# Kernel optimization log

Measured on AMD Instinct MI355X. Metric: run time of the kernel, lower is better.

## Reference

```python
import jax, jax.numpy as jnp
import numpy as np

DMODEL = 512
NUM_HEADS = 8
DK = DMODEL // NUM_HEADS  # 64
CAUSAL = True


def setup_inputs() -> dict:
    key = jax.random.key(0)
    ks = jax.random.split(key, 11)
    B, S = 4, 2048
    s_in = 1.0 / np.sqrt(DMODEL)
    s_out = 1.0 / np.sqrt(NUM_HEADS * DK)
    return {
        "Q": jax.random.normal(ks[0], (B, S, DMODEL), jnp.float32),
        "K": jax.random.normal(ks[1], (B, S, DMODEL), jnp.float32),
        "V": jax.random.normal(ks[2], (B, S, DMODEL), jnp.float32),
        # torch nn.Linear weights stored as [in, out] (already transposed)
        "WQ_w": jax.random.uniform(ks[3], (DMODEL, DK), jnp.float32, -s_in, s_in),
        "WQ_b": jax.random.uniform(ks[4], (DK,), jnp.float32, -s_in, s_in),
        "WK_w": jax.random.uniform(ks[5], (DMODEL, DK), jnp.float32, -s_in, s_in),
        "WK_b": jax.random.uniform(ks[6], (DK,), jnp.float32, -s_in, s_in),
        "WV_w": jax.random.uniform(ks[7], (DMODEL, DK), jnp.float32, -s_in, s_in),
        "WV_b": jax.random.uniform(ks[8], (DK,), jnp.float32, -s_in, s_in),
        "Wo_w": jax.random.uniform(ks[9], (NUM_HEADS * DK, DMODEL), jnp.float32, -s_out, s_out),
        "Wo_b": jax.random.uniform(ks[10], (DMODEL,), jnp.float32, -s_out, s_out),
    }


def reference(Q, K, V, WQ_w, WQ_b, WK_w, WK_b, WV_w, WV_b, Wo_w, Wo_b):
    # Single shared projection to dk=64 (NOT per-head in the original module)
    q = Q @ WQ_w + WQ_b  # [B,S,dk]
    k = K @ WK_w + WK_b  # [B,S,dk]
    v = V @ WV_w + WV_b  # [B,S,dk]
    scores = jnp.einsum("bsd,btd->bst", q, k) / np.sqrt(DK).astype(np.float32)
    if CAUSAL:
        S = scores.shape[-1]
        causal = jnp.tril(jnp.ones((S, S), dtype=bool))  # True = keep
        scores = jnp.where(causal, scores, -jnp.inf)
    attn = jax.nn.softmax(scores, axis=-1)
    head_out = jnp.einsum("bst,btd->bsd", attn, v)  # [B,S,dk]
    # Every head is identical -> concat == tile num_heads copies
    concat = jnp.tile(head_out, (1, 1, NUM_HEADS))  # [B,S,num_heads*dk]
    return concat @ Wo_w + Wo_b  # [B,S,dmodel]
```

## Files before the change

### kernel.cpp

```cpp
#include <hip/hip_runtime.h>
#include <hip/hip_bf16.h>

#define DMODEL 512
#define DK 64
#define NH 8
#define SEQ 2048
#define BATCH 4
#define NROWS 8192
#define NEGBIG -1.0e30f
#define SPLITW 8
#define DKP 66

typedef _Float16 half_t;
typedef _Float16 half8 __attribute__((ext_vector_type(8)));
typedef _Float16 half4 __attribute__((ext_vector_type(4)));
typedef _Float16 half2v __attribute__((ext_vector_type(2)));
typedef float floatx4 __attribute__((ext_vector_type(4)));

#if defined(__has_builtin)
#if __has_builtin(__builtin_amdgcn_mfma_f32_16x16x16f16)
#define HAVE_MFMA16X16X16 1
#else
#define HAVE_MFMA16X16X16 0
#endif
#else
#define HAVE_MFMA16X16X16 0
#endif

__device__ __forceinline__ float expc(float x) { return __expf(fmaxf(x, -80.0f)); }

__global__ __launch_bounds__(256) void prep_kernel(
    const float* __restrict__ WQ, const float* __restrict__ WK,
    const float* __restrict__ WV, const float* __restrict__ Wo,
    half_t* __restrict__ wtq, half_t* __restrict__ wtk, half_t* __restrict__ wtv,
    float* __restrict__ woe)
{
    const int idx = blockIdx.x * 256 + threadIdx.x;
    const int n = idx >> 9;
    const int k = idx & 511;
    wtq[idx] = (half_t)WQ[k * DK + n];
    wtk[idx] = (half_t)WK[k * DK + n];
    wtv[idx] = (half_t)WV[k * DK + n];
    float s = 0.f;
#pragma unroll
    for (int h = 0; h < NH; h++)
        s += Wo[((size_t)(h * DK + n)) * DMODEL + k];
    woe[idx] = s;
}

__global__ __launch_bounds__(64) void proj_kernel(
    const float* __restrict__ Q, const float* __restrict__ K, const float* __restrict__ V,
    const half_t* __restrict__ wtq, const half_t* __restrict__ wtk, const half_t* __restrict__ wtv,
    const float* __restrict__ bQ, const float* __restrict__ bK, const float* __restrict__ bV,
    half_t* __restrict__ qh, half_t* __restrict__ kh, half_t* __restrict__ vt)
{
    const int tens = blockIdx.y;
    const float* X  = (tens == 0) ? Q : (tens == 1) ? K : V;
    const half_t* wt = (tens == 0) ? wtq : (tens == 1) ? wtk : wtv;
    const float* bias = (tens == 0) ? bQ : (tens == 1) ? bK : bV;

    const int r0 = blockIdx.x * 16;
    const int lane = threadIdx.x;
    const int c = lane & 15;
    const int quad = lane >> 4;

    floatx4 acc[4] = {{0.f,0.f,0.f,0.f},{0.f,0.f,0.f,0.f},{0.f,0.f,0.f,0.f},{0.f,0.f,0.f,0.f}};

    const float* xrow = X + (size_t)(r0 + c) * DMODEL + quad * 8;
#pragma unroll 8
    for (int ks = 0; ks < 16; ks++) {
        const float* xp = xrow + ks * 32;
        half8 a;
#pragma unroll
        for (int i = 0; i < 8; i++) a[i] = (half_t)xp[i];
#pragma unroll
        for (int nt = 0; nt < 4; nt++) {
            half8 bfr = *(const half8*)(wt + (size_t)(nt * 16 + c) * DMODEL + ks * 32 + quad * 8);
            acc[nt] = __builtin_amdgcn_mfma_f32_16x16x32_f16(a, bfr, acc[nt], 0, 0, 0);
        }
    }

#pragma unroll
    for (int nt = 0; nt < 4; nt++) {
        const float bv = bias[nt * 16 + c];
#pragma unroll
        for (int r = 0; r < 4; r++) {
            const float val = acc[nt][r] + bv;
            const int row = r0 + quad * 4 + r;
            if (tens == 0) {
                qh[(size_t)row * DK + nt * 16 + c] = (half_t)val;
            } else if (tens == 1) {
                kh[(size_t)row * DK + nt * 16 + c] = (half_t)val;
            } else {
                const int b  = row >> 11;
                const int s  = row & (SEQ - 1);
                const int kb = s >> 4;
                const int kk = s & 15;
                vt[((((size_t)b * 128 + kb) * 4 + nt) * 16 + c) * 16 + kk] = (half_t)val;
            }
        }
    }
}

__global__ __launch_bounds__(512, 4) void attn_kernel(
    const half_t* __restrict__ qh, const half_t* __restrict__ kh,
    const half_t* __restrict__ vt, half_t* __restrict__ hof)
{
    const int bx = blockIdx.x;
    const int b = bx >> 7;
    const int qt = bx & 127;
    const int tid = threadIdx.x;
    const int w = tid >> 6;
    const int lane = tid & 63;
    const int c = lane & 15;
    const int quad = lane >> 4;

    __shared__ float sow[SPLITW][16][DKP];
    __shared__ float sm_s[SPLITW][16];
    __shared__ float sl_s[SPLITW][16];

    const half_t* qrow = qh + (size_t)(b * SEQ + qt * 16 + c) * DK + quad * 8;
    half8 qb0 = *(const half8*)(qrow);
    half8 qb1 = *(const half8*)(qrow + 32);
#pragma unroll
    for (int i = 0; i < 8; i++) { qb0[i] = qb0[i] * (half_t)0.125f; qb1[i] = qb1[i] * (half_t)0.125f; }

    float m = NEGBIG, l = 0.f;
    floatx4 o[4] = {{0.f,0.f,0.f,0.f},{0.f,0.f,0.f,0.f},{0.f,0.f,0.f,0.f},{0.f,0.f,0.f,0.f}};

    const half_t* kbb = kh + (size_t)b * SEQ * DK;
    const half_t* vtb = vt + (size_t)b * 128 * 1024;

    int kb = w;
    half8 ka0, ka1;
    if (kb <= qt) {
        const half_t* krow = kbb + (size_t)(kb * 16 + c) * DK + quad * 8;
        ka0 = *(const half8*)(krow);
        ka1 = *(const half8*)(krow + 32);
    }

    while (kb <= qt) {
        const half_t* vkb = vtb + (size_t)kb * 1024;
#if HAVE_MFMA16X16X16
        half4 vb0 = *(const half4*)(vkb + ((size_t)0 * 16 + c) * 16 + quad * 4);
        half4 vb1 = *(const half4*)(vkb + ((size_t)1 * 16 + c) * 16 + quad * 4);
        half4 vb2 = *(const half4*)(vkb + ((size_t)2 * 16 + c) * 16 + quad * 4);
        half4 vb3 = *(const half4*)(vkb + ((size_t)3 * 16 + c) * 16 + quad * 4);
#else
        half8 vb80 = *(const half8*)(vkb + ((size_t)0 * 16 + c) * 16 + (quad & 1) * 8);
        half8 vb81 = *(const half8*)(vkb + ((size_t)1 * 16 + c) * 16 + (quad & 1) * 8);
        half8 vb82 = *(const half8*)(vkb + ((size_t)2 * 16 + c) * 16 + (quad & 1) * 8);
        half8 vb83 = *(const half8*)(vkb + ((size_t)3 * 16 + c) * 16 + (quad & 1) * 8);
#endif
        const int nkb = kb + SPLITW;
        half8 nka0 = ka0, nka1 = ka1;
        if (nkb <= qt) {
            const half_t* nkrow = kbb + (size_t)(nkb * 16 + c) * DK + quad * 8;
            nka0 = *(const half8*)(nkrow);
            nka1 = *(const half8*)(nkrow + 32);
        }

        floatx4 sc = {0.f, 0.f, 0.f, 0.f};
        sc = __builtin_amdgcn_mfma_f32_16x16x32_f16(ka0, qb0, sc, 0, 0, 0);
        sc = __builtin_amdgcn_mfma_f32_16x16x32_f16(ka1, qb1, sc, 0, 0, 0);

        if (kb == qt) {
#pragma unroll
            for (int r = 0; r < 4; r++)
                if (quad * 4 + r > c) sc[r] = NEGBIG;
        }

        float tm = fmaxf(fmaxf(sc[0], sc[1]), fmaxf(sc[2], sc[3]));
        tm = fmaxf(tm, __shfl_xor(tm, 16));
        tm = fmaxf(tm, __shfl_xor(tm, 32));
        const float mn = fmaxf(m, tm);
        const float alpha = expc(m - mn);
        float p[4];
#pragma unroll
        for (int r = 0; r < 4; r++) p[r] = expc(sc[r] - mn);
        float ts = p[0] + p[1] + p[2] + p[3];
        ts += __shfl_xor(ts, 16);
        ts += __shfl_xor(ts, 32);
        l = l * alpha + ts;
        m = mn;

        const float a0 = __shfl(alpha, quad * 4 + 0);
        const float a1 = __shfl(alpha, quad * 4 + 1);
        const float a2 = __shfl(alpha, quad * 4 + 2);
        const float a3 = __shfl(alpha, quad * 4 + 3);
#pragma unroll
        for (int nt = 0; nt < 4; nt++) {
            o[nt][0] *= a0; o[nt][1] *= a1; o[nt][2] *= a2; o[nt][3] *= a3;
        }

#if HAVE_MFMA16X16X16
        half4 pa;
#pragma unroll
        for (int r = 0; r < 4; r++) pa[r] = (half_t)p[r];
        o[0] = __builtin_amdgcn_mfma_f32_16x16x16f16(pa, vb0, o[0], 0, 0, 0);
        o[1] = __builtin_amdgcn_mfma_f32_16x16x16f16(pa, vb1, o[1], 0, 0, 0);
        o[2] = __builtin_amdgcn_mfma_f32_16x16x16f16(pa, vb2, o[2], 0, 0, 0);
        o[3] = __builtin_amdgcn_mfma_f32_16x16x16f16(pa, vb3, o[3], 0, 0, 0);
#else
        half8 pa8;
#pragma unroll
        for (int j = 0; j < 8; j++) {
            const int src = (((quad * 2 + (j >> 2)) & 3) * 16 + c);
            const float pj = __shfl(p[j & 3], src);
            pa8[j] = (quad < 2) ? (half_t)pj : (half_t)0.f;
        }
        o[0] = __builtin_amdgcn_mfma_f32_16x16x32_f16(pa8, vb80, o[0], 0, 0, 0);
        o[1] = __builtin_amdgcn_mfma_f32_16x16x32_f16(pa8, vb81, o[1], 0, 0, 0);
        o[2] = __builtin_amdgcn_mfma_f32_16x16x32_f16(pa8, vb82, o[2], 0, 0, 0);
        o[3] = __builtin_amdgcn_mfma_f32_16x16x32_f16(pa8, vb83, o[3], 0, 0, 0);
#endif
        ka0 = nka0; ka1 = nka1; kb = nkb;
    }

#pragma unroll
    for (int nt = 0; nt < 4; nt++)
#pragma unroll
        for (int r = 0; r < 4; r++)
            sow[w][quad * 4 + r][nt * 16 + c] = o[nt][r];
    if (quad == 0) { sm_s[w][c] = m; sl_s[w][c] = l; }
    __syncthreads();

    const int q = w * 2 + (lane >> 5);
    const int d0 = (lane & 31) * 2;
    float mstar = NEGBIG;
#pragma unroll
    for (int ww = 0; ww < SPLITW; ww++) mstar = fmaxf(mstar, sm_s[ww][q]);
    float lstar = 0.f, acc0 = 0.f, acc1 = 0.f;
#pragma unroll
    for (int ww = 0; ww < SPLITW; ww++) {
        const float beta = expc(sm_s[ww][q] - mstar);
        lstar += beta * sl_s[ww][q];
        const float* sp = &sow[ww][q][d0];
        acc0 += beta * sp[0];
        acc1 += beta * sp[1];
    }
    const float linv = 1.f / lstar;
    half2v res;
    res[0] = (half_t)(acc0 * linv);
    res[1] = (half_t)(acc1 * linv);
    *(half2v*)(hof + (size_t)(b * SEQ + qt * 16 + q) * DK + d0) = res;
}

__global__ __launch_bounds__(256) void out_kernel(
    const half_t* __restrict__ ho, const float* __restrict__ woe,
    const float* __restrict__ bo, float* __restrict__ out)
{
    const int r0 = blockIdx.x * 8;
    const int t = threadIdx.x;
    __shared__ float hs[8][DK];
    {
        const int rr = t >> 5, cc = (t & 31) * 2;
        hs[rr][cc]     = (float)ho[(size_t)(r0 + rr) * DK + cc];
        hs[rr][cc + 1] = (float)ho[(size_t)(r0 + rr) * DK + cc + 1];
    }
    __syncthreads();

    float acc[8][2] = {};
#pragma unroll 4
    for (int i = 0; i < DK; i++) {
        const float w0 = woe[i * DMODEL + t];
        const float w1 = woe[i * DMODEL + t + 256];
#pragma unroll
        for (int r = 0; r < 8; r++) {
            const float h = hs[r][i];
            acc[r][0] += h * w0;
            acc[r][1] += h * w1;
        }
    }
    const float b0 = bo[t], b1 = bo[t + 256];
#pragma unroll
    for (int r = 0; r < 8; r++) {
        out[(size_t)(r0 + r) * DMODEL + t]       = acc[r][0] + b0;
        out[(size_t)(r0 + r) * DMODEL + t + 256] = acc[r][1] + b1;
    }
}

extern "C" void kernel_launch(void* const* d_in, const int* in_sizes, int n_in,
                              void* d_out, int out_size, void* d_ws, size_t ws_size,
                              hipStream_t stream) {
    const float* Q  = (const float*)d_in[0];
    const float* K  = (const float*)d_in[1];
    const float* V  = (const float*)d_in[2];
    const float* WQ = (const float*)d_in[3];
    const float* bQ = (const float*)d_in[4];
    const float* WK = (const float*)d_in[5];
    const float* bK = (const float*)d_in[6];
    const float* WV = (const float*)d_in[7];
    const float* bV = (const float*)d_in[8];
    const float* Wo = (const float*)d_in[9];
    const float* bo = (const float*)d_in[10];
    float* out = (float*)d_out;

    char* ws = (char*)d_ws;
    half_t* qh  = (half_t*)ws;
    half_t* kh  = (half_t*)(ws + (1u << 20));
    half_t* vt  = (half_t*)(ws + (2u << 20));
    half_t* hof = (half_t*)(ws + (3u << 20));
    half_t* wtq = hof;
    half_t* wtk = wtq + 32768;
    half_t* wtv = wtk + 32768;
    float*  woe = (float*)(ws + (4u << 20));

    prep_kernel<<<128, 256, 0, stream>>>(WQ, WK, WV, Wo, wtq, wtk, wtv, woe);
    proj_kernel<<<dim3(512, 3), 64, 0, stream>>>(Q, K, V, wtq, wtk, wtv, bQ, bK, bV, qh, kh, vt);
    attn_kernel<<<512, 512, 0, stream>>>(qh, kh, vt, hof);
    out_kernel<<<1024, 256, 0, stream>>>(hof, woe, bo, out);
}
```

Measured before the change: 156.2 us.

## Fuse output projection into attention epilogue via MFMA and split projection K-loop

The separate fp32 output-projection kernel is removed. Each attention block now writes its normalized 16x64 head output to LDS and multiplies it by a transposed, head-summed fp16 Wo with MFMA, adding the bias and storing fp32 output directly. This drops the intermediate global round-trip and one launch. The projection kernel also splits its K loop across two wavefronts with an LDS reduction for more parallelism. In exchange, Wo is quantized to fp16.

```diff
diff --git a/kernel.cpp b/kernel.cpp
--- a/kernel.cpp
+++ b/kernel.cpp
@@ -33,7 +33,7 @@
     const float* __restrict__ WQ, const float* __restrict__ WK,
     const float* __restrict__ WV, const float* __restrict__ Wo,
     half_t* __restrict__ wtq, half_t* __restrict__ wtk, half_t* __restrict__ wtv,
-    float* __restrict__ woe)
+    half_t* __restrict__ wo_tr)
 {
     const int idx = blockIdx.x * 256 + threadIdx.x;
     const int n = idx >> 9;
@@ -41,14 +41,16 @@
     wtq[idx] = (half_t)WQ[k * DK + n];
     wtk[idx] = (half_t)WK[k * DK + n];
     wtv[idx] = (half_t)WV[k * DK + n];
+    const int n2 = idx >> 6;
+    const int k2 = idx & 63;
     float s = 0.f;
 #pragma unroll
     for (int h = 0; h < NH; h++)
-        s += Wo[((size_t)(h * DK + n)) * DMODEL + k];
-    woe[idx] = s;
+        s += Wo[((size_t)(h * DK + k2)) * DMODEL + n2];
+    wo_tr[idx] = (half_t)s;
 }
 
-__global__ __launch_bounds__(64) void proj_kernel(
+__global__ __launch_bounds__(128) void proj_kernel(
     const float* __restrict__ Q, const float* __restrict__ K, const float* __restrict__ V,
     const half_t* __restrict__ wtq, const half_t* __restrict__ wtk, const half_t* __restrict__ wtv,
     const float* __restrict__ bQ, const float* __restrict__ bK, const float* __restrict__ bV,
@@ -60,15 +62,19 @@
     const float* bias = (tens == 0) ? bQ : (tens == 1) ? bK : bV;
 
     const int r0 = blockIdx.x * 16;
-    const int lane = threadIdx.x;
+    const int tid = threadIdx.x;
+    const int w = tid >> 6;
+    const int lane = tid & 63;
     const int c = lane & 15;
     const int quad = lane >> 4;
 
+    __shared__ floatx4 red[4][64];
+
     floatx4 acc[4] = {{0.f,0.f,0.f,0.f},{0.f,0.f,0.f,0.f},{0.f,0.f,0.f,0.f},{0.f,0.f,0.f,0.f}};
 
     const float* xrow = X + (size_t)(r0 + c) * DMODEL + quad * 8;
 #pragma unroll 8
-    for (int ks = 0; ks < 16; ks++) {
+    for (int ks = w; ks < 16; ks += 2) {
         const float* xp = xrow + ks * 32;
         half8 a;
 #pragma unroll
@@ -80,12 +86,20 @@
         }
     }
 
+    if (w == 1) {
+#pragma unroll
+        for (int nt = 0; nt < 4; nt++) red[nt][lane] = acc[nt];
+    }
+    __syncthreads();
+    if (w == 1) return;
+
 #pragma unroll
     for (int nt = 0; nt < 4; nt++) {
+        const floatx4 r4 = red[nt][lane];
         const float bv = bias[nt * 16 + c];
 #pragma unroll
         for (int r = 0; r < 4; r++) {
-            const float val = acc[nt][r] + bv;
+            const float val = acc[nt][r] + r4[r] + bv;
             const int row = r0 + quad * 4 + r;
             if (tens == 0) {
                 qh[(size_t)row * DK + nt * 16 + c] = (half_t)val;
@@ -104,7 +118,8 @@
 
 __global__ __launch_bounds__(512, 4) void attn_kernel(
     const half_t* __restrict__ qh, const half_t* __restrict__ kh,
-    const half_t* __restrict__ vt, half_t* __restrict__ hof)
+    const half_t* __restrict__ vt, const half_t* __restrict__ wo_tr,
+    const float* __restrict__ bo, float* __restrict__ out)
 {
     const int bx = blockIdx.x;
     const int b = bx >> 7;
@@ -118,6 +133,7 @@
     __shared__ float sow[SPLITW][16][DKP];
     __shared__ float sm_s[SPLITW][16];
     __shared__ float sl_s[SPLITW][16];
+    __shared__ half_t of16[16][72];
 
     const half_t* qrow = qh + (size_t)(b * SEQ + qt * 16 + c) * DK + quad * 8;
     half8 qb0 = *(const half8*)(qrow);
@@ -225,58 +241,42 @@
     if (quad == 0) { sm_s[w][c] = m; sl_s[w][c] = l; }
     __syncthreads();
 
-    const int q = w * 2 + (lane >> 5);
-    const int d0 = (lane & 31) * 2;
-    float mstar = NEGBIG;
-#pragma unroll
-    for (int ww = 0; ww < SPLITW; ww++) mstar = fmaxf(mstar, sm_s[ww][q]);
-    float lstar = 0.f, acc0 = 0.f, acc1 = 0.f;
-#pragma unroll
-    for (int ww = 0; ww < SPLITW; ww++) {
-        const float beta = expc(sm_s[ww][q] - mstar);
-        lstar += beta * sl_s[ww][q];
-        const float* sp = &sow[ww][q][d0];
-        acc0 += beta * sp[0];
-        acc1 += beta * sp[1];
-    }
-    const float linv = 1.f / lstar;
-    half2v res;
-    res[0] = (half_t)(acc0 * linv);
-    res[1] = (half_t)(acc1 * linv);
-    *(half2v*)(hof + (size_t)(b * SEQ + qt * 16 + q) * DK + d0) = res;
-}
-
-__global__ __launch_bounds__(256) void out_kernel(
-    const half_t* __restrict__ ho, const float* __restrict__ woe,
-    const float* __restrict__ bo, float* __restrict__ out)
-{
-    const int r0 = blockIdx.x * 8;
-    const int t = threadIdx.x;
-    __shared__ float hs[8][DK];
     {
-        const int rr = t >> 5, cc = (t & 31) * 2;
-        hs[rr][cc]     = (float)ho[(size_t)(r0 + rr) * DK + cc];
-        hs[rr][cc + 1] = (float)ho[(size_t)(r0 + rr) * DK + cc + 1];
+        const int q = w * 2 + (lane >> 5);
+        const int d0 = (lane & 31) * 2;
+        float mstar = NEGBIG;
+#pragma unroll
+        for (int ww = 0; ww < SPLITW; ww++) mstar = fmaxf(mstar, sm_s[ww][q]);
+        float lstar = 0.f, acc0 = 0.f, acc1 = 0.f;
+#pragma unroll
+        for (int ww = 0; ww < SPLITW; ww++) {
+            const float beta = expc(sm_s[ww][q] - mstar);
+            lstar += beta * sl_s[ww][q];
+            const float* sp = &sow[ww][q][d0];
+            acc0 += beta * sp[0];
+            acc1 += beta * sp[1];
+        }
+        const float linv = 1.f / lstar;
+        of16[q][d0]     = (half_t)(acc0 * linv);
+        of16[q][d0 + 1] = (half_t)(acc1 * linv);
     }
     __syncthreads();
 
-    float acc[8][2] = {};
-#pragma unroll 4
-    for (int i = 0; i < DK; i++) {
-        const float w0 = woe[i * DMODEL + t];
-        const float w1 = woe[i * DMODEL + t + 256];
-#pragma unroll
-        for (int r = 0; r < 8; r++) {
-            const float h = hs[r][i];
-            acc[r][0] += h * w0;
-            acc[r][1] += h * w1;
-        }
-    }
-    const float b0 = bo[t], b1 = bo[t + 256];
-#pragma unroll
-    for (int r = 0; r < 8; r++) {
-        out[(size_t)(r0 + r) * DMODEL + t]       = acc[r][0] + b0;
-        out[(size_t)(r0 + r) * DMODEL + t + 256] = acc[r][1] + b1;
+    half8 a1 = *(const half8*)(&of16[c][quad * 8]);
+    half8 a2 = *(const half8*)(&of16[c][32 + quad * 8]);
+    const size_t orow = (size_t)(b * SEQ + qt * 16);
+#pragma unroll
+    for (int i = 0; i < 4; i++) {
+        const int n = (w * 4 + i) * 16 + c;
+        half8 b1 = *(const half8*)(wo_tr + (size_t)n * DK + quad * 8);
+        half8 b2 = *(const half8*)(wo_tr + (size_t)n * DK + 32 + quad * 8);
+        floatx4 oc = {0.f, 0.f, 0.f, 0.f};
+        oc = __builtin_amdgcn_mfma_f32_16x16x32_f16(a1, b1, oc, 0, 0, 0);
+        oc = __builtin_amdgcn_mfma_f32_16x16x32_f16(a2, b2, oc, 0, 0, 0);
+        const float bv = bo[n];
+#pragma unroll
+        for (int r = 0; r < 4; r++)
+            out[(orow + quad * 4 + r) * DMODEL + n] = oc[r] + bv;
     }
 }
 
@@ -297,17 +297,15 @@
     float* out = (float*)d_out;
 
     char* ws = (char*)d_ws;
-    half_t* qh  = (half_t*)ws;
-    half_t* kh  = (half_t*)(ws + (1u << 20));
-    half_t* vt  = (half_t*)(ws + (2u << 20));
-    half_t* hof = (half_t*)(ws + (3u << 20));
-    half_t* wtq = hof;
-    half_t* wtk = wtq + 32768;
-    half_t* wtv = wtk + 32768;
-    float*  woe = (float*)(ws + (4u << 20));
-
-    prep_kernel<<<128, 256, 0, stream>>>(WQ, WK, WV, Wo, wtq, wtk, wtv, woe);
-    proj_kernel<<<dim3(512, 3), 64, 0, stream>>>(Q, K, V, wtq, wtk, wtv, bQ, bK, bV, qh, kh, vt);
-    attn_kernel<<<512, 512, 0, stream>>>(qh, kh, vt, hof);
-    out_kernel<<<1024, 256, 0, stream>>>(hof, woe, bo, out);
+    half_t* qh    = (half_t*)ws;
+    half_t* kh    = (half_t*)(ws + (1u << 20));
+    half_t* vt    = (half_t*)(ws + (2u << 20));
+    half_t* wtq   = (half_t*)(ws + (3u << 20));
+    half_t* wtk   = wtq + 32768;
+    half_t* wtv   = wtk + 32768;
+    half_t* wo_tr = wtv + 32768;
+
+    prep_kernel<<<128, 256, 0, stream>>>(WQ, WK, WV, Wo, wtq, wtk, wtv, wo_tr);
+    proj_kernel<<<dim3(512, 3), 128, 0, stream>>>(Q, K, V, wtq, wtk, wtv, bQ, bK, bV, qh, kh, vt);
+    attn_kernel<<<512, 512, 0, stream>>>(qh, kh, vt, wo_tr, bo, out);
 }
```

After: 150.3 us. 1.04x faster.
